# Performance work log

Measured on AMD Instinct MI355X. Metric: run time of the kernel, lower is better.

## Reference

```python
import jax, jax.numpy as jnp
import numpy as np

B, S, D, H, L = 32, 512, 256, 8, 3
HD = D // H
FFN = D // 2
SCALE_BASE = 512.0
EPS = 1e-5


def _gammas():
    return (1.0 - jnp.exp(jnp.linspace(np.log(1.0 / 32.0), np.log(1.0 / 512.0), H))).astype(jnp.float32)


def _xpos(x, downscale):
    # x: [..., S, hd]; XPOS rotary embedding with exponential length scaling
    s, hd = x.shape[-2], x.shape[-1]
    half = hd // 2
    scale = (jnp.arange(0, hd, 2, dtype=jnp.float32) + 0.4 * hd) / (1.4 * hd)  # [half]
    power = jnp.arange(s, dtype=jnp.float32)[:, None] / SCALE_BASE
    sm = scale[None, :] ** power  # [S, half]
    if downscale:
        sm = 1.0 / sm
    inv_freq = 1.0 / (10000.0 ** (jnp.arange(half, dtype=jnp.float32) / half))
    ang = jnp.arange(s, dtype=jnp.float32)[:, None] * inv_freq[None, :]  # [S, half]
    sin = jnp.repeat(jnp.sin(ang) * sm, 2, axis=-1)  # duplicate_interleave -> [S, hd]
    cos = jnp.repeat(jnp.cos(ang) * sm, 2, axis=-1)
    x1, x2 = x[..., ::2], x[..., 1::2]
    rot = jnp.stack((-x2, x1), axis=-1).reshape(x.shape)  # rotate_every_two
    return x * cos + rot * sin


def _layer_norm(x, w, b):
    mu = x.mean(-1, keepdims=True)
    var = ((x - mu) ** 2).mean(-1, keepdims=True)
    return (x - mu) / jnp.sqrt(var + EPS) * w + b


def _msr(X, WQ, WK, WV, WG, WO, gn_w, gn_b):
    # Multi-scale retention, parallel form. X: [B,S,D]; WQ/WK/WV: [H,D,HD]
    b, s, _ = X.shape
    Q = _xpos(jnp.einsum('bsd,hde->bhse', X, WQ), False)
    K = _xpos(jnp.einsum('bsd,hde->bhse', X, WK), True)
    V = jnp.einsum('bsd,hde->bhse', X, WV)
    n = jnp.arange(s)
    delta = (n[:, None] - n[None, :]).astype(jnp.float32)
    mask = n[:, None] >= n[None, :]
    g = _gammas()
    Dm = jnp.where(mask[None], g[:, None, None] ** delta[None], 0.0)  # [H,S,S]
    scores = jnp.einsum('bhse,bhte->bhst', Q, K) * Dm[None]  # [B,H,S,S]
    Y = jnp.einsum('bhst,bhte->bhse', scores, V)  # [B,H,S,HD]
    Y = jnp.moveaxis(Y, 1, 2)  # [B,S,H,HD] (= concat heads)
    # GroupNorm(heads, v_dim): normalize per (token, head) group
    mu = Y.mean(-1, keepdims=True)
    var = ((Y - mu) ** 2).mean(-1, keepdims=True)
    Yn = ((Y - mu) / jnp.sqrt(var + EPS)).reshape(b, s, D) * gn_w + gn_b
    G = X @ WG
    return (G * jax.nn.sigmoid(G) * Yn) @ WO


def setup_inputs() -> dict:
    key = jax.random.key(0)
    ks = jax.random.split(key, 10)
    inp = {
        'v': jax.random.randint(ks[0], (B, S), 0, 65, dtype=jnp.int64),
        'emb': jax.random.normal(ks[1], (65, D), dtype=jnp.float32),
        'WQ': jax.random.normal(ks[2], (L, H, D, HD), dtype=jnp.float32) / D,
        'WK': jax.random.normal(ks[3], (L, H, D, HD), dtype=jnp.float32) / D,
        'WV': jax.random.normal(ks[4], (L, H, D, HD), dtype=jnp.float32) / D,
        'WG': jax.random.normal(ks[5], (L, D, D), dtype=jnp.float32) / D,
        'WO': jax.random.normal(ks[6], (L, D, D), dtype=jnp.float32) / D,
        'gn_w': jnp.ones((L, D), jnp.float32),
        'gn_b': jnp.zeros((L, D), jnp.float32),
        'ln1_w': jnp.ones((L, D), jnp.float32),
        'ln1_b': jnp.zeros((L, D), jnp.float32),
        'ln2_w': jnp.ones((L, D), jnp.float32),
        'ln2_b': jnp.zeros((L, D), jnp.float32),
        'w1': jax.random.normal(ks[7], (L, D, FFN), dtype=jnp.float32) * (1.0 / np.sqrt(D)),
        'b1': jnp.zeros((L, FFN), jnp.float32),
        'w2': jax.random.normal(ks[8], (L, FFN, D), dtype=jnp.float32) * (1.0 / np.sqrt(FFN)),
        'b2': jnp.zeros((L, D), jnp.float32),
    }
    return inp


def reference(v, emb, WQ, WK, WV, WG, WO, gn_w, gn_b, ln1_w, ln1_b, ln2_w, ln2_b, w1, b1, w2, b2):
    emb = emb.at[0].set(0.0)  # padding_idx=0
    X = jax.nn.relu(emb[v])  # [B,S,D]
    for i in range(L):
        Y = _msr(_layer_norm(X, ln1_w[i], ln1_b[i]), WQ[i], WK[i], WV[i], WG[i], WO[i], gn_w[i], gn_b[i]) + X
        h = jax.nn.gelu(_layer_norm(Y, ln2_w[i], ln2_b[i]) @ w1[i] + b1[i], approximate=False)
        X = h @ w2[i] + b2[i] + Y
    return X
```

## Files before the change

### kernel.cpp

```cpp
#include <hip/hip_runtime.h>
#include <hip/hip_bf16.h>
#include <math.h>

#define BB 32
#define SS 512
#define DD 256
#define HH 8
#define HDIM 32
#define FFNN 128
#define NROWS (BB*SS)
#define NELEM (NROWS*DD)

using bf16 = __hip_bfloat16;
typedef __attribute__((ext_vector_type(8))) short short8;
typedef __attribute__((ext_vector_type(4))) short short4v;
typedef __attribute__((ext_vector_type(4))) float floatx4;
typedef unsigned int uint_al __attribute__((may_alias));

static __device__ __forceinline__ float bf2f(bf16 x) { return __bfloat162float(x); }
static __device__ __forceinline__ bf16  f2bf(float x) { return __float2bfloat16(x); }
static __device__ __forceinline__ short f2bfs(float x) {
    bf16 b = __float2bfloat16(x);
    return __builtin_bit_cast(short, b);
}

static __device__ __forceinline__ unsigned int cvtpk(float a, float b) {
    unsigned int r;
    asm("v_cvt_pk_bf16_f32 %0, %1, %2" : "=v"(r) : "v"(a), "v"(b));
    return r;
}
static __device__ __forceinline__ short4v mk4(unsigned int a, unsigned int b) {
    union { unsigned int u[2]; short4v s; } t;
    t.u[0] = a; t.u[1] = b;
    return t.s;
}
static __device__ __forceinline__ floatx4 mfma16(short4v a, short4v b, floatx4 c) {
#if __has_builtin(__builtin_amdgcn_mfma_f32_16x16x16bf16_1k)
    return __builtin_amdgcn_mfma_f32_16x16x16bf16_1k(a, b, c, 0, 0, 0);
#else
    asm("v_mfma_f32_16x16x16_bf16 %0, %1, %2, %0" : "+v"(c) : "v"(a), "v"(b));
    return c;
#endif
}

static __device__ __forceinline__ void gld_lds16(const void* g, void* l) {
    __builtin_amdgcn_global_load_lds(
        (const __attribute__((address_space(1))) void*)g,
        (__attribute__((address_space(3))) void*)l, 16, 0, 0);
}

__global__ void init_flag(int* flag) { *flag = 0; }
__global__ __launch_bounds__(256) void detect_v(const int* __restrict__ v, int* __restrict__ flag) {
    int i = blockIdx.x * 256 + threadIdx.x;
    if (v[2 * i + 1] != 0) atomicOr(flag, 1);
}

#define NQKVG (3*1024*256)
#define NWO   (3*256*256)
#define NW1   (3*128*256)
#define NW2   (3*256*128)
#define NXPT  (512*16)
#define NSETUP (NQKVG+NWO+NW1+NW2+NXPT)
__global__ __launch_bounds__(256) void setup_pack(const float* __restrict__ WQ, const float* __restrict__ WK,
                                                  const float* __restrict__ WV, const float* __restrict__ WG,
                                                  const float* __restrict__ WO, const float* __restrict__ w1,
                                                  const float* __restrict__ w2,
                                                  bf16* __restrict__ dQ, bf16* __restrict__ dO,
                                                  bf16* __restrict__ d1, bf16* __restrict__ d2,
                                                  float4* __restrict__ xpt) {
    int idx = blockIdx.x * 256 + threadIdx.x;
    if (idx < NQKVG) {
        int k = idx & 255, n = (idx >> 8) & 1023, l = idx >> 18;
        int seg = n >> 8, n8 = n & 255;
        float val;
        if (seg < 3) {
            const float* W = (seg == 0) ? WQ : (seg == 1) ? WK : WV;
            int h = n8 >> 5, e = n8 & 31;
            val = W[(((size_t)l * 8 + h) * 256 + k) * 32 + e];
        } else {
            val = WG[(size_t)l * 65536 + k * 256 + n8];
        }
        dQ[((size_t)l * 1024 + n) * 256 + k] = f2bf(val);
    } else if (idx < NQKVG + NWO) {
        int i = idx - NQKVG;
        int k = i & 255, n = (i >> 8) & 255, l = i >> 16;
        dO[((size_t)l * 256 + n) * 256 + k] = f2bf(WO[(size_t)l * 65536 + k * 256 + n]);
    } else if (idx < NQKVG + NWO + NW1) {
        int i = idx - NQKVG - NWO;
        int k = i & 255, n = (i >> 8) & 127, l = i >> 15;
        d1[((size_t)l * 128 + n) * 256 + k] = f2bf(w1[(size_t)l * 32768 + k * 128 + n]);
    } else if (idx < NQKVG + NWO + NW1 + NW2) {
        int i = idx - NQKVG - NWO - NW1;
        int k = i & 127, n = (i >> 7) & 255, l = i >> 15;
        d2[((size_t)l * 256 + n) * 128 + k] = f2bf(w2[(size_t)l * 32768 + k * 256 + n]);
    } else {
        int i = idx - NQKVG - NWO - NW1 - NW2;
        int jf = i & 15, s = i >> 4;
        float base = (2.0f * jf + 12.8f) / 44.8f;
        float sm = powf(base, (float)s * (1.0f / 512.0f));
        float ang = (float)s * powf(10000.0f, -(float)jf / 16.0f);
        float sn, cs;
        sincosf(ang, &sn, &cs);
        xpt[i] = float4{cs * sm, sn * sm, cs / sm, sn / sm};
    }
}

__global__ __launch_bounds__(256) void embed_ln_kernel(const int* __restrict__ v,
                                                       const float* __restrict__ emb,
                                                       const int* __restrict__ flag,
                                                       const float* __restrict__ w,
                                                       const float* __restrict__ b,
                                                       float* __restrict__ X,
                                                       short* __restrict__ Xn) {
    int row = blockIdx.x;
    int d = threadIdx.x;
    int tok = (*flag) ? v[row] : v[2 * row];
    float x = 0.0f;
    if (tok != 0) {
        x = emb[tok * DD + d];
        x = x > 0.0f ? x : 0.0f;
    }
    X[(size_t)row * DD + d] = x;
    float s1 = x, s2 = x * x;
    #pragma unroll
    for (int off = 1; off < 64; off <<= 1) {
        s1 += __shfl_xor(s1, off);
        s2 += __shfl_xor(s2, off);
    }
    __shared__ float p1[4], p2[4], st[2];
    int wid = threadIdx.x >> 6;
    if ((threadIdx.x & 63) == 0) { p1[wid] = s1; p2[wid] = s2; }
    __syncthreads();
    if (threadIdx.x == 0) {
        float t1 = p1[0] + p1[1] + p1[2] + p1[3];
        float t2 = p2[0] + p2[1] + p2[2] + p2[3];
        float mu = t1 * (1.0f / DD);
        float var = t2 * (1.0f / DD) - mu * mu;
        st[0] = mu; st[1] = rsqrtf(var + 1e-5f);
    }
    __syncthreads();
    Xn[(size_t)row * DD + d] = f2bfs((x - st[0]) * st[1] * w[d] + b[d]);
}

__global__ __launch_bounds__(256) void qkvg_gemm(const short* __restrict__ A,
                                                 const short* __restrict__ Bp,
                                                 const float4* __restrict__ xpt,
                                                 bf16* __restrict__ C) {
    __shared__ __align__(16) short Als[16 * 512];
    __shared__ __align__(16) short Bls[16 * 512];
    const int tid = threadIdx.x;
    const int wave = tid >> 6, lane = tid & 63, lo = lane & 15, quad = lane >> 4;
    const int wm = wave >> 1, wn = wave & 1;
    const int row0 = blockIdx.x * 128, col0 = blockIdx.y * 128;

    floatx4 acc[4][4];
    #pragma unroll
    for (int i = 0; i < 4; ++i)
        #pragma unroll
        for (int j = 0; j < 4; ++j) acc[i][j] = floatx4{0.f, 0.f, 0.f, 0.f};

    for (int k0 = 0; k0 < 256; k0 += 64) {
        #pragma unroll
        for (int t = 0; t < 4; ++t) {
            int grp = (wm * 4 + t) * 2 + wn;
            const short* ga = A + (size_t)(row0 + (wm * 4 + t) * 16 + lo) * 256
                            + k0 + (wn * 4 + quad) * 8;
            gld_lds16(ga, &Als[grp * 512]);
        }
        #pragma unroll
        for (int t = 0; t < 4; ++t) {
            int grp = (wn * 4 + t) * 2 + wm;
            const short* gb = Bp + (size_t)(col0 + (wn * 4 + t) * 16 + lo) * 256
                            + k0 + (wm * 4 + quad) * 8;
            gld_lds16(gb, &Bls[grp * 512]);
        }
        __syncthreads();
        #pragma unroll
        for (int kkgrp = 0; kkgrp < 2; ++kkgrp) {
            short8 af[4], bfr[4];
            #pragma unroll
            for (int t = 0; t < 4; ++t)
                af[t] = *(const short8*)(&Als[((wm * 4 + t) * 2 + kkgrp) * 512 + lane * 8]);
            #pragma unroll
            for (int t = 0; t < 4; ++t)
                bfr[t] = *(const short8*)(&Bls[((wn * 4 + t) * 2 + kkgrp) * 512 + lane * 8]);
            #pragma unroll
            for (int ti = 0; ti < 4; ++ti)
                #pragma unroll
                for (int tj = 0; tj < 4; ++tj)
                    acc[ti][tj] = __builtin_amdgcn_mfma_f32_16x16x32_bf16(af[ti], bfr[tj], acc[ti][tj], 0, 0, 0);
        }
        __syncthreads();
    }

    #pragma unroll
    for (int ti = 0; ti < 4; ++ti) {
        #pragma unroll
        for (int tj = 0; tj < 4; ++tj) {
            int colb = col0 + (wn * 4 + tj) * 16 + lo;
            int seg = colb >> 8;
            #pragma unroll
            for (int r = 0; r < 4; ++r) {
                int row = row0 + (wm * 4 + ti) * 16 + quad * 4 + r;
                float v = acc[ti][tj][r];
                if (seg < 2) {
                    int s = row & (SS - 1);
                    int jf = (colb & 31) >> 1;
                    float4 t = xpt[s * 16 + jf];
                    float cs = (seg == 0) ? t.x : t.z;
                    float sn = (seg == 0) ? t.y : t.w;
                    float p = __shfl_xor(v, 1);
                    v = (lo & 1) ? (v * cs + p * sn) : (v * cs - p * sn);
                }
                C[(size_t)row * 1024 + colb] = f2bf(v);
            }
        }
    }
}

__global__ __launch_bounds__(256) void wo_gemm(const short* __restrict__ A,
                                               const short* __restrict__ Bp,
                                               float* __restrict__ X,
                                               const float* __restrict__ lnw,
                                               const float* __restrict__ lnb,
                                               short* __restrict__ Out) {
    __shared__ __align__(16) short Als[4 * 512];
    __shared__ __align__(16) short Bls[4][8 * 512];
    __shared__ float Ssum[32][4], Ssq[32][4];
    const int tid = threadIdx.x;
    const int wave = tid >> 6, lane = tid & 63, lo = lane & 15, quad = lane >> 4;
    const int row0 = blockIdx.x * 32;
    const int colw0 = wave * 64;

    floatx4 acc[2][4];
    #pragma unroll
    for (int i = 0; i < 2; ++i)
        #pragma unroll
        for (int j = 0; j < 4; ++j) acc[i][j] = floatx4{0.f, 0.f, 0.f, 0.f};

    const short* Ab = A + (size_t)(row0 + (wave >> 1) * 16 + lo) * 1024 + ((wave & 1) * 4 + quad) * 8;
    const short* Bb = Bp + (size_t)(colw0 + lo) * 256 + quad * 8;

    for (int k0 = 0; k0 < 256; k0 += 64) {
        gld_lds16(Ab + k0, &Als[wave * 512]);
        #pragma unroll
        for (int t = 0; t < 4; ++t)
            #pragma unroll
            for (int kk = 0; kk < 2; ++kk)
                gld_lds16(Bb + (size_t)(t * 16) * 256 + k0 + kk * 32,
                          &Bls[wave][(t * 2 + kk) * 512]);
        __syncthreads();
        #pragma unroll
        for (int kk = 0; kk < 2; ++kk) {
            short8 af[2], bfr[4];
            #pragma unroll
            for (int t = 0; t < 2; ++t)
                af[t] = *(const short8*)(&Als[(t * 2 + kk) * 512 + lane * 8]);
            #pragma unroll
            for (int t = 0; t < 4; ++t)
                bfr[t] = *(const short8*)(&Bls[wave][(t * 2 + kk) * 512 + lane * 8]);
            #pragma unroll
            for (int ti = 0; ti < 2; ++ti)
                #pragma unroll
                for (int tj = 0; tj < 4; ++tj)
                    acc[ti][tj] = __builtin_amdgcn_mfma_f32_16x16x32_bf16(af[ti], bfr[tj], acc[ti][tj], 0, 0, 0);
        }
        __syncthreads();
    }

    float vv[2][4][4];
    #pragma unroll
    for (int ti = 0; ti < 2; ++ti)
        #pragma unroll
        for (int tj = 0; tj < 4; ++tj) {
            int colb = colw0 + tj * 16 + lo;
            #pragma unroll
            for (int r = 0; r < 4; ++r) {
                int row = row0 + ti * 16 + quad * 4 + r;
                float v = acc[ti][tj][r] + X[(size_t)row * DD + colb];
                X[(size_t)row * DD + colb] = v;
                vv[ti][tj][r] = v;
            }
        }
    #pragma unroll
    for (int ti = 0; ti < 2; ++ti)
        #pragma unroll
        for (int r = 0; r < 4; ++r) {
            float s1 = 0.f, s2 = 0.f;
            #pragma unroll
            for (int tj = 0; tj < 4; ++tj) {
                float v = vv[ti][tj][r];
                s1 += v; s2 += v * v;
            }
            #pragma unroll
            for (int off = 1; off < 16; off <<= 1) {
                s1 += __shfl_xor(s1, off);
                s2 += __shfl_xor(s2, off);
            }
            if (lo == 0) {
                int rl = ti * 16 + quad * 4 + r;
                Ssum[rl][wave] = s1;
                Ssq[rl][wave] = s2;
            }
        }
    __syncthreads();
    #pragma unroll
    for (int ti = 0; ti < 2; ++ti)
        #pragma unroll
        for (int r = 0; r < 4; ++r) {
            int rl = ti * 16 + quad * 4 + r;
            float t1 = Ssum[rl][0] + Ssum[rl][1] + Ssum[rl][2] + Ssum[rl][3];
            float t2 = Ssq[rl][0] + Ssq[rl][1] + Ssq[rl][2] + Ssq[rl][3];
            float mu = t1 * (1.0f / DD);
            float var = t2 * (1.0f / DD) - mu * mu;
            float rs = rsqrtf(var + 1e-5f);
            int row = row0 + rl;
            #pragma unroll
            for (int tj = 0; tj < 4; ++tj) {
                int colb = colw0 + tj * 16 + lo;
                Out[(size_t)row * DD + colb] =
                    f2bfs((vv[ti][tj][r] - mu) * rs * lnw[colb] + lnb[colb]);
            }
        }
}

#define HSTR 136
template<int DOLN>
__global__ __launch_bounds__(256) void ffn_fused(const short* __restrict__ Xn,
                                                 const short* __restrict__ W1p,
                                                 const float* __restrict__ b1,
                                                 const short* __restrict__ W2p,
                                                 const float* __restrict__ b2,
                                                 float* __restrict__ X,
                                                 const float* __restrict__ lnw,
                                                 const float* __restrict__ lnb,
                                                 short* __restrict__ Out) {
    __shared__ __align__(16) short Als[4 * 512];
    __shared__ __align__(16) short Bls[4][8 * 512];
    __shared__ __align__(16) short Hls[32 * HSTR];
    __shared__ float Ssum[32][4], Ssq[32][4];
    const int tid = threadIdx.x;
    const int wave = tid >> 6, lane = tid & 63, lo = lane & 15, quad = lane >> 4;
    const int row0 = blockIdx.x * 32;

    floatx4 a1[2][2];
    #pragma unroll
    for (int i = 0; i < 2; ++i) { a1[i][0] = floatx4{0,0,0,0}; a1[i][1] = floatx4{0,0,0,0}; }
    const short* Ab = Xn + (size_t)(row0 + (wave >> 1) * 16 + lo) * 256 + ((wave & 1) * 4 + quad) * 8;
    const short* Bb1 = W1p + (size_t)(wave * 32 + lo) * 256 + quad * 8;
    for (int k0 = 0; k0 < 256; k0 += 64) {
        gld_lds16(Ab + k0, &Als[wave * 512]);
        #pragma unroll
        for (int t = 0; t < 2; ++t)
            #pragma unroll
            for (int kk = 0; kk < 2; ++kk)
                gld_lds16(Bb1 + (size_t)(t * 16) * 256 + k0 + kk * 32,
                          &Bls[wave][(t * 2 + kk) * 512]);
        __syncthreads();
        #pragma unroll
        for (int kk = 0; kk < 2; ++kk) {
            short8 af[2], bfr[2];
            #pragma unroll
            for (int t = 0; t < 2; ++t)
                af[t] = *(const short8*)(&Als[(t * 2 + kk) * 512 + lane * 8]);
            #pragma unroll
            for (int t = 0; t < 2; ++t)
                bfr[t] = *(const short8*)(&Bls[wave][(t * 2 + kk) * 512 + lane * 8]);
            #pragma unroll
            for (int ti = 0; ti < 2; ++ti)
                #pragma unroll
                for (int tj = 0; tj < 2; ++tj)
                    a1[ti][tj] = __builtin_amdgcn_mfma_f32_16x16x32_bf16(af[ti], bfr[tj], a1[ti][tj], 0, 0, 0);
        }
        __syncthreads();
    }
    #pragma unroll
    for (int ti = 0; ti < 2; ++ti)
        #pragma unroll
        for (int tj = 0; tj < 2; ++tj) {
            int colb = wave * 32 + tj * 16 + lo;
            float bs = b1[colb];
            #pragma unroll
            for (int r = 0; r < 4; ++r) {
                int rl = ti * 16 + quad * 4 + r;
                float v = a1[ti][tj][r] + bs;
                v = 0.5f * v * (1.0f + erff(v * 0.70710678118f));
                Hls[rl * HSTR + colb] = f2bfs(v);
            }
        }

    floatx4 a2[2][4];
    #pragma unroll
    for (int i = 0; i < 2; ++i)
        #pragma unroll
        for (int j = 0; j < 4; ++j) a2[i][j] = floatx4{0,0,0,0};
    const short* Bb2 = W2p + (size_t)(wave * 64 + lo) * 128 + quad * 8;
    for (int k0 = 0; k0 < 128; k0 += 64) {
        #pragma unroll
        for (int t = 0; t < 4; ++t)
            #pragma unroll
            for (int kk = 0; kk < 2; ++kk)
                gld_lds16(Bb2 + (size_t)(t * 16) * 128 + k0 + kk * 32,
                          &Bls[wave][(t * 2 + kk) * 512]);
        __syncthreads();
        #pragma unroll
        for (int kk = 0; kk < 2; ++kk) {
            short8 af[2], bfr[4];
            #pragma unroll
            for (int t = 0; t < 2; ++t)
                af[t] = *(const short8*)(&Hls[(t * 16 + lo) * HSTR + k0 + kk * 32 + quad * 8]);
            #pragma unroll
            for (int t = 0; t < 4; ++t)
                bfr[t] = *(const short8*)(&Bls[wave][(t * 2 + kk) * 512 + lane * 8]);
            #pragma unroll
            for (int ti = 0; ti < 2; ++ti)
                #pragma unroll
                for (int tj = 0; tj < 4; ++tj)
                    a2[ti][tj] = __builtin_amdgcn_mfma_f32_16x16x32_bf16(af[ti], bfr[tj], a2[ti][tj], 0, 0, 0);
        }
        __syncthreads();
    }

    float vv[2][4][4];
    #pragma unroll
    for (int ti = 0; ti < 2; ++ti)
        #pragma unroll
        for (int tj = 0; tj < 4; ++tj) {
            int colb = wave * 64 + tj * 16 + lo;
            float bs = b2[colb];
            #pragma unroll
            for (int r = 0; r < 4; ++r) {
                int row = row0 + ti * 16 + quad * 4 + r;
                float v = a2[ti][tj][r] + bs + X[(size_t)row * DD + colb];
                X[(size_t)row * DD + colb] = v;
                vv[ti][tj][r] = v;
            }
        }
    if (!DOLN) return;
    #pragma unroll
    for (int ti = 0; ti < 2; ++ti)
        #pragma unroll
        for (int r = 0; r < 4; ++r) {
            float s1 = 0.f, s2 = 0.f;
            #pragma unroll
            for (int tj = 0; tj < 4; ++tj) {
                float v = vv[ti][tj][r];
                s1 += v; s2 += v * v;
            }
            #pragma unroll
            for (int off = 1; off < 16; off <<= 1) {
                s1 += __shfl_xor(s1, off);
                s2 += __shfl_xor(s2, off);
            }
            if (lo == 0) {
                int rl = ti * 16 + quad * 4 + r;
                Ssum[rl][wave] = s1;
                Ssq[rl][wave] = s2;
            }
        }
    __syncthreads();
    #pragma unroll
    for (int ti = 0; ti < 2; ++ti)
        #pragma unroll
        for (int r = 0; r < 4; ++r) {
            int rl = ti * 16 + quad * 4 + r;
            float t1 = Ssum[rl][0] + Ssum[rl][1] + Ssum[rl][2] + Ssum[rl][3];
            float t2 = Ssq[rl][0] + Ssq[rl][1] + Ssq[rl][2] + Ssq[rl][3];
            float mu = t1 * (1.0f / DD);
            float var = t2 * (1.0f / DD) - mu * mu;
            float rs = rsqrtf(var + 1e-5f);
            int row = row0 + rl;
            #pragma unroll
            for (int tj = 0; tj < 4; ++tj) {
                int colb = wave * 64 + tj * 16 + lo;
                Out[(size_t)row * DD + colb] =
                    f2bfs((vv[ti][tj][r] - mu) * rs * lnw[colb] + lnb[colb]);
            }
        }
}

#define VSTR 44
__global__ __launch_bounds__(256) void retention_mfma_kernel(bf16* __restrict__ QKVG,
                                                             const float* __restrict__ gnw,
                                                             const float* __restrict__ gnb) {
    __shared__ __align__(16) short Vt[4][32 * VSTR];
    const int wslot = threadIdx.x >> 6;
    const int lane = threadIdx.x & 63;
    const int gblk = blockIdx.x >> 6;
    const int qi = 15 - ((gblk & ~3) + (((gblk & 3) + (gblk >> 2)) & 3));
    const int bh = ((blockIdx.x & 63) << 2) | wslot;
    const int b = bh >> 3, h = bh & 7;
    const int q0 = qi * 32;
    const int lo = lane & 15, quad = lane >> 4;

    const float la0 = -3.46573590280f, la1 = -6.23832462504f;
    float gamma = 1.0f - expf(la0 + (float)h * (la1 - la0) / 7.0f);
    float lg2 = log2f(gamma);
    float g16i = exp2f(-16.0f * lg2);
    float g16p = exp2f(16.0f * lg2);
    float gi32 = exp2f(-32.0f * lg2);
    float wq[4], wq16[4], wqB[4];
    #pragma unroll
    for (int r = 0; r < 4; ++r) {
        wq[r]   = exp2f((float)(lo - 4 * quad - r) * lg2);
        wq16[r] = wq[r] * g16i;
        wqB[r]  = wq[r] * g16p;
    }
    float c = exp2f((float)q0 * lg2);

    const size_t base = (size_t)b * SS * 1024;
    const short* QKVGs = (const short*)QKVG;

    short8 qfA = *(const short8*)(QKVGs + base + (size_t)(q0 + lo) * 1024 + h * HDIM + quad * 8);
    short8 qfB = *(const short8*)(QKVGs + base + (size_t)(q0 + 16 + lo) * 1024 + h * HDIM + quad * 8);

    floatx4 oA0 = {0,0,0,0}, oA1 = {0,0,0,0}, oB0 = {0,0,0,0}, oB1 = {0,0,0,0};
    short* Vw = Vt[wslot];
    const int nch = qi + 1;

    for (int ch = 0; ch < nch; ++ch) {
        const int t0 = ch * 32;
        const short* Kb = QKVGs + base + 256 + h * HDIM + quad * 8;
        short8 kf0 = *(const short8*)(Kb + (size_t)(t0 + lo) * 1024);
        short8 kf1 = *(const short8*)(Kb + (size_t)(t0 + 16 + lo) * 1024);
        {
            const int r = lane >> 2, dcol = (lane & 3) * 8;
            const short* Vg = QKVGs + base + 512 + h * HDIM + dcol;
            uint4 u1 = *(const uint4*)(Vg + (size_t)(t0 + r) * 1024);
            uint4 u2 = *(const uint4*)(Vg + (size_t)(t0 + 16 + r) * 1024);
            uint_al* W1 = (uint_al*)(Vw + r * VSTR + dcol);
            uint_al* W2 = (uint_al*)(Vw + (16 + r) * VSTR + dcol);
            W1[0] = u1.x; W1[1] = u1.y; W1[2] = u1.z; W1[3] = u1.w;
            W2[0] = u2.x; W2[1] = u2.y; W2[2] = u2.z; W2[3] = u2.w;
        }
        const floatx4 z = {0,0,0,0};
        floatx4 sA0 = __builtin_amdgcn_mfma_f32_16x16x32_bf16(kf0, qfA, z, 0, 0, 0);
        floatx4 sA1 = __builtin_amdgcn_mfma_f32_16x16x32_bf16(kf1, qfA, z, 0, 0, 0);
        floatx4 sB0 = __builtin_amdgcn_mfma_f32_16x16x32_bf16(kf0, qfB, z, 0, 0, 0);
        floatx4 sB1 = __builtin_amdgcn_mfma_f32_16x16x32_bf16(kf1, qfB, z, 0, 0, 0);

        float m0[4], m1[4], mB[4];
        #pragma unroll
        for (int r = 0; r < 4; ++r) {
            m0[r] = c * wq[r];
            m1[r] = c * wq16[r];
            mB[r] = c * wqB[r];
        }
        if (ch == qi) {
            #pragma unroll
            for (int r = 0; r < 4; ++r) {
                if (lo < 4 * quad + r) m0[r] = 0.0f;
                m1[r] = 0.0f;
            }
        }
        c *= gi32;

        unsigned int pa0 = cvtpk(sA0[0] * m0[0], sA0[1] * m0[1]);
        unsigned int pa1 = cvtpk(sA0[2] * m0[2], sA0[3] * m0[3]);
        unsigned int pa2 = cvtpk(sA1[0] * m1[0], sA1[1] * m1[1]);
        unsigned int pa3 = cvtpk(sA1[2] * m1[2], sA1[3] * m1[3]);
        unsigned int pb0 = cvtpk(sB0[0] * mB[0], sB0[1] * mB[1]);
        unsigned int pb1 = cvtpk(sB0[2] * mB[2], sB0[3] * mB[3]);
        unsigned int pb2 = cvtpk(sB1[0] * m0[0], sB1[1] * m0[1]);
        unsigned int pb3 = cvtpk(sB1[2] * m0[2], sB1[3] * m0[3]);
        short4v pA0 = mk4(pa0, pa1), pA1 = mk4(pa2, pa3);
        short4v pB0 = mk4(pb0, pb1), pB1 = mk4(pb2, pb3);

        short4v v00, v01, v10, v11;
        #pragma unroll
        for (int j = 0; j < 4; ++j) {
            v00[j] = Vw[(4 * quad + j) * VSTR + lo];
            v01[j] = Vw[(16 + 4 * quad + j) * VSTR + lo];
            v10[j] = Vw[(4 * quad + j) * VSTR + 16 + lo];
            v11[j] = Vw[(16 + 4 * quad + j) * VSTR + 16 + lo];
        }
        oA0 = mfma16(pA0, v00, oA0);
        oA0 = mfma16(pA1, v01, oA0);
        oA1 = mfma16(pA0, v10, oA1);
        oA1 = mfma16(pA1, v11, oA1);
        oB0 = mfma16(pB0, v00, oB0);
        oB0 = mfma16(pB1, v01, oB0);
        oB1 = mfma16(pB0, v10, oB1);
        oB1 = mfma16(pB1, v11, oB1);
    }

    float gw0 = gnw[h * HDIM + lo], gw1 = gnw[h * HDIM + 16 + lo];
    float gb0 = gnb[h * HDIM + lo], gb1 = gnb[h * HDIM + 16 + lo];
    bf16* QK = QKVG;
    #pragma unroll
    for (int sub = 0; sub < 2; ++sub) {
        floatx4 o0 = sub ? oB0 : oA0;
        floatx4 o1 = sub ? oB1 : oA1;
        int qbase = q0 + sub * 16;
        #pragma unroll
        for (int r = 0; r < 4; ++r) {
            float y0 = o0[r], y1 = o1[r];
            float s = y0 + y1, ss = y0 * y0 + y1 * y1;
            #pragma unroll
            for (int off = 1; off < 16; off <<= 1) {
                s  += __shfl_xor(s, off);
                ss += __shfl_xor(ss, off);
            }
            float mu = s * (1.0f / HDIM);
            float var = ss * (1.0f / HDIM) - mu * mu;
            float rstd = rsqrtf(var + 1e-5f);
            int q = qbase + quad * 4 + r;
            size_t rowb = base + (size_t)q * 1024;
            float g0 = bf2f(QK[rowb + 768 + h * HDIM + lo]);
            float g1 = bf2f(QK[rowb + 768 + h * HDIM + 16 + lo]);
            float t0v = g0 / (1.0f + expf(-g0)) * ((y0 - mu) * rstd * gw0 + gb0);
            float t1v = g1 / (1.0f + expf(-g1)) * ((y1 - mu) * rstd * gw1 + gb1);
            QK[rowb + h * HDIM + lo]      = f2bf(t0v);
            QK[rowb + h * HDIM + 16 + lo] = f2bf(t1v);
        }
    }
}

extern "C" void kernel_launch(void* const* d_in, const int* in_sizes, int n_in,
                              void* d_out, int out_size, void* d_ws, size_t ws_size,
                              hipStream_t stream) {
    const int*   v    = (const int*)d_in[0];
    const float* emb  = (const float*)d_in[1];
    const float* WQ   = (const float*)d_in[2];
    const float* WK   = (const float*)d_in[3];
    const float* WV   = (const float*)d_in[4];
    const float* WG   = (const float*)d_in[5];
    const float* WO   = (const float*)d_in[6];
    const float* gn_w = (const float*)d_in[7];
    const float* gn_b = (const float*)d_in[8];
    const float* ln1w = (const float*)d_in[9];
    const float* ln1b = (const float*)d_in[10];
    const float* ln2w = (const float*)d_in[11];
    const float* ln2b = (const float*)d_in[12];
    const float* w1   = (const float*)d_in[13];
    const float* b1   = (const float*)d_in[14];
    const float* w2   = (const float*)d_in[15];
    const float* b2   = (const float*)d_in[16];

    float* X = (float*)d_out;

    float* base  = (float*)d_ws;
    int*   flag  = (int*)base;
    short* Xn    = (short*)(base + 16);
    bf16*  QKVG  = (bf16*)(Xn + (size_t)NROWS * 256);
    bf16*  WqkvgP = QKVG + (size_t)NROWS * 1024;
    bf16*  WoP   = WqkvgP + 3 * 1024 * 256;
    bf16*  W1P   = WoP + 3 * 256 * 256;
    bf16*  W2P   = W1P + 3 * 128 * 256;
    float4* xpt  = (float4*)(W2P + 3 * 256 * 128);

    init_flag<<<1, 1, 0, stream>>>(flag);
    detect_v<<<32, 256, 0, stream>>>(v, flag);
    setup_pack<<<NSETUP / 256, 256, 0, stream>>>(WQ, WK, WV, WG, WO, w1, w2,
                                                 WqkvgP, WoP, W1P, W2P, xpt);
    embed_ln_kernel<<<NROWS, 256, 0, stream>>>(v, emb, flag, ln1w, ln1b, X, Xn);

    for (int i = 0; i < 3; ++i) {
        qkvg_gemm<<<dim3(128, 8), 256, 0, stream>>>(Xn,
                                                    (const short*)(WqkvgP + (size_t)i * 1024 * 256),
                                                    xpt, QKVG);
        retention_mfma_kernel<<<1024, 256, 0, stream>>>(QKVG, gn_w + i * DD, gn_b + i * DD);
        wo_gemm<<<NROWS / 32, 256, 0, stream>>>((const short*)QKVG,
                                                (const short*)(WoP + (size_t)i * 256 * 256),
                                                X, ln2w + i * DD, ln2b + i * DD, Xn);
        if (i < 2)
            ffn_fused<1><<<NROWS / 32, 256, 0, stream>>>(Xn,
                                                         (const short*)(W1P + (size_t)i * 128 * 256),
                                                         b1 + i * FFNN,
                                                         (const short*)(W2P + (size_t)i * 256 * 128),
                                                         b2 + i * DD, X,
                                                         ln1w + (i + 1) * DD, ln1b + (i + 1) * DD, Xn);
        else
            ffn_fused<0><<<NROWS / 32, 256, 0, stream>>>(Xn,
                                                         (const short*)(W1P + (size_t)i * 128 * 256),
                                                         b1 + i * FFNN,
                                                         (const short*)(W2P + (size_t)i * 256 * 128),
                                                         b2 + i * DD, X,
                                                         nullptr, nullptr, nullptr);
    }
}
```

Baseline: 396.4 us.

## Fuse WO projection, LayerNorm and FFN into one kernel per layer

Merges the WO GEMM kernel and the FFN kernel into a single kernel per row block. The post-residual LayerNorm output stays in LDS as the FFN input, and the residual stays in registers. This removes one launch per layer, the global round trip of the normalized activations, and a reread of X. In exchange, LDS use per block grows (an extra 32x264 bf16 buffer) and register pressure rises, which may lower occupancy.

```diff
diff --git a/kernel.cpp b/kernel.cpp
--- a/kernel.cpp
+++ b/kernel.cpp
@@ -218,14 +218,25 @@
     }
 }
 
-__global__ __launch_bounds__(256) void wo_gemm(const short* __restrict__ A,
-                                               const short* __restrict__ Bp,
-                                               float* __restrict__ X,
-                                               const float* __restrict__ lnw,
-                                               const float* __restrict__ lnb,
-                                               short* __restrict__ Out) {
+#define HS2 264
+#define HSTR 136
+template<int DOLN>
+__global__ __launch_bounds__(256) void wo_ffn_fused(const short* __restrict__ A,
+                                                    const short* __restrict__ Wo,
+                                                    const short* __restrict__ W1p,
+                                                    const float* __restrict__ b1,
+                                                    const short* __restrict__ W2p,
+                                                    const float* __restrict__ b2,
+                                                    float* __restrict__ X,
+                                                    const float* __restrict__ ln2w,
+                                                    const float* __restrict__ ln2b,
+                                                    const float* __restrict__ ln1w,
+                                                    const float* __restrict__ ln1b,
+                                                    short* __restrict__ Xn) {
     __shared__ __align__(16) short Als[4 * 512];
     __shared__ __align__(16) short Bls[4][8 * 512];
+    __shared__ __align__(16) short Hn[32 * HS2];
+    __shared__ __align__(16) short Hf[32 * HSTR];
     __shared__ float Ssum[32][4], Ssq[32][4];
     const int tid = threadIdx.x;
     const int wave = tid >> 6, lane = tid & 63, lo = lane & 15, quad = lane >> 4;
@@ -239,7 +250,7 @@
         for (int j = 0; j < 4; ++j) acc[i][j] = floatx4{0.f, 0.f, 0.f, 0.f};
 
     const short* Ab = A + (size_t)(row0 + (wave >> 1) * 16 + lo) * 1024 + ((wave & 1) * 4 + quad) * 8;
-    const short* Bb = Bp + (size_t)(colw0 + lo) * 256 + quad * 8;
+    const short* Bb = Wo + (size_t)(colw0 + lo) * 256 + quad * 8;
 
     for (int k0 = 0; k0 < 256; k0 += 64) {
         gld_lds16(Ab + k0, &Als[wave * 512]);
@@ -277,11 +288,141 @@
             #pragma unroll
             for (int r = 0; r < 4; ++r) {
                 int row = row0 + ti * 16 + quad * 4 + r;
-                float v = acc[ti][tj][r] + X[(size_t)row * DD + colb];
+                vv[ti][tj][r] = acc[ti][tj][r] + X[(size_t)row * DD + colb];
+            }
+        }
+    #pragma unroll
+    for (int ti = 0; ti < 2; ++ti)
+        #pragma unroll
+        for (int r = 0; r < 4; ++r) {
+            float s1 = 0.f, s2 = 0.f;
+            #pragma unroll
+            for (int tj = 0; tj < 4; ++tj) {
+                float v = vv[ti][tj][r];
+                s1 += v; s2 += v * v;
+            }
+            #pragma unroll
+            for (int off = 1; off < 16; off <<= 1) {
+                s1 += __shfl_xor(s1, off);
+                s2 += __shfl_xor(s2, off);
+            }
+            if (lo == 0) {
+                int rl = ti * 16 + quad * 4 + r;
+                Ssum[rl][wave] = s1;
+                Ssq[rl][wave] = s2;
+            }
+        }
+    __syncthreads();
+    #pragma unroll
+    for (int ti = 0; ti < 2; ++ti)
+        #pragma unroll
+        for (int r = 0; r < 4; ++r) {
+            int rl = ti * 16 + quad * 4 + r;
+            float t1 = Ssum[rl][0] + Ssum[rl][1] + Ssum[rl][2] + Ssum[rl][3];
+            float t2 = Ssq[rl][0] + Ssq[rl][1] + Ssq[rl][2] + Ssq[rl][3];
+            float mu = t1 * (1.0f / DD);
+            float var = t2 * (1.0f / DD) - mu * mu;
+            float rs = rsqrtf(var + 1e-5f);
+            #pragma unroll
+            for (int tj = 0; tj < 4; ++tj) {
+                int colb = colw0 + tj * 16 + lo;
+                Hn[rl * HS2 + colb] =
+                    f2bfs((vv[ti][tj][r] - mu) * rs * ln2w[colb] + ln2b[colb]);
+            }
+        }
+    __syncthreads();
+
+    floatx4 a1[2][2];
+    #pragma unroll
+    for (int i = 0; i < 2; ++i) { a1[i][0] = floatx4{0,0,0,0}; a1[i][1] = floatx4{0,0,0,0}; }
+    const short* Bb1 = W1p + (size_t)(wave * 32 + lo) * 256 + quad * 8;
+    for (int k0 = 0; k0 < 256; k0 += 64) {
+        #pragma unroll
+        for (int t = 0; t < 2; ++t)
+            #pragma unroll
+            for (int kk = 0; kk < 2; ++kk)
+                gld_lds16(Bb1 + (size_t)(t * 16) * 256 + k0 + kk * 32,
+                          &Bls[wave][(t * 2 + kk) * 512]);
+        __syncthreads();
+        #pragma unroll
+        for (int kk = 0; kk < 2; ++kk) {
+            short8 af[2], bfr[2];
+            #pragma unroll
+            for (int t = 0; t < 2; ++t)
+                af[t] = *(const short8*)(&Hn[(t * 16 + lo) * HS2 + k0 + kk * 32 + quad * 8]);
+            #pragma unroll
+            for (int t = 0; t < 2; ++t)
+                bfr[t] = *(const short8*)(&Bls[wave][(t * 2 + kk) * 512 + lane * 8]);
+            #pragma unroll
+            for (int ti = 0; ti < 2; ++ti)
+                #pragma unroll
+                for (int tj = 0; tj < 2; ++tj)
+                    a1[ti][tj] = __builtin_amdgcn_mfma_f32_16x16x32_bf16(af[ti], bfr[tj], a1[ti][tj], 0, 0, 0);
+        }
+        __syncthreads();
+    }
+    #pragma unroll
+    for (int ti = 0; ti < 2; ++ti)
+        #pragma unroll
+        for (int tj = 0; tj < 2; ++tj) {
+            int colb = wave * 32 + tj * 16 + lo;
+            float bs = b1[colb];
+            #pragma unroll
+            for (int r = 0; r < 4; ++r) {
+                int rl = ti * 16 + quad * 4 + r;
+                float v = a1[ti][tj][r] + bs;
+                v = 0.5f * v * (1.0f + erff(v * 0.70710678118f));
+                Hf[rl * HSTR + colb] = f2bfs(v);
+            }
+        }
+
+    floatx4 a2[2][4];
+    #pragma unroll
+    for (int i = 0; i < 2; ++i)
+        #pragma unroll
+        for (int j = 0; j < 4; ++j) a2[i][j] = floatx4{0,0,0,0};
+    const short* Bb2 = W2p + (size_t)(colw0 + lo) * 128 + quad * 8;
+    for (int k0 = 0; k0 < 128; k0 += 64) {
+        #pragma unroll
+        for (int t = 0; t < 4; ++t)
+            #pragma unroll
+            for (int kk = 0; kk < 2; ++kk)
+                gld_lds16(Bb2 + (size_t)(t * 16) * 128 + k0 + kk * 32,
+                          &Bls[wave][(t * 2 + kk) * 512]);
+        __syncthreads();
+        #pragma unroll
+        for (int kk = 0; kk < 2; ++kk) {
+            short8 af[2], bfr[4];
+            #pragma unroll
+            for (int t = 0; t < 2; ++t)
+                af[t] = *(const short8*)(&Hf[(t * 16 + lo) * HSTR + k0 + kk * 32 + quad * 8]);
+            #pragma unroll
+            for (int t = 0; t < 4; ++t)
+                bfr[t] = *(const short8*)(&Bls[wave][(t * 2 + kk) * 512 + lane * 8]);
+            #pragma unroll
+            for (int ti = 0; ti < 2; ++ti)
+                #pragma unroll
+                for (int tj = 0; tj < 4; ++tj)
+                    a2[ti][tj] = __builtin_amdgcn_mfma_f32_16x16x32_bf16(af[ti], bfr[tj], a2[ti][tj], 0, 0, 0);
+        }
+        __syncthreads();
+    }
+
+    #pragma unroll
+    for (int ti = 0; ti < 2; ++ti)
+        #pragma unroll
+        for (int tj = 0; tj < 4; ++tj) {
+            int colb = colw0 + tj * 16 + lo;
+            float bs = b2[colb];
+            #pragma unroll
+            for (int r = 0; r < 4; ++r) {
+                int row = row0 + ti * 16 + quad * 4 + r;
+                float v = a2[ti][tj][r] + bs + vv[ti][tj][r];
                 X[(size_t)row * DD + colb] = v;
                 vv[ti][tj][r] = v;
             }
         }
+    if (!DOLN) return;
     #pragma unroll
     for (int ti = 0; ti < 2; ++ti)
         #pragma unroll
@@ -318,163 +459,8 @@
             #pragma unroll
             for (int tj = 0; tj < 4; ++tj) {
                 int colb = colw0 + tj * 16 + lo;
-                Out[(size_t)row * DD + colb] =
-                    f2bfs((vv[ti][tj][r] - mu) * rs * lnw[colb] + lnb[colb]);
-            }
-        }
-}
-
-#define HSTR 136
-template<int DOLN>
-__global__ __launch_bounds__(256) void ffn_fused(const short* __restrict__ Xn,
-                                                 const short* __restrict__ W1p,
-                                                 const float* __restrict__ b1,
-                                                 const short* __restrict__ W2p,
-                                                 const float* __restrict__ b2,
-                                                 float* __restrict__ X,
-                                                 const float* __restrict__ lnw,
-                                                 const float* __restrict__ lnb,
-                                                 short* __restrict__ Out) {
-    __shared__ __align__(16) short Als[4 * 512];
-    __shared__ __align__(16) short Bls[4][8 * 512];
-    __shared__ __align__(16) short Hls[32 * HSTR];
-    __shared__ float Ssum[32][4], Ssq[32][4];
-    const int tid = threadIdx.x;
-    const int wave = tid >> 6, lane = tid & 63, lo = lane & 15, quad = lane >> 4;
-    const int row0 = blockIdx.x * 32;
-
-    floatx4 a1[2][2];
-    #pragma unroll
-    for (int i = 0; i < 2; ++i) { a1[i][0] = floatx4{0,0,0,0}; a1[i][1] = floatx4{0,0,0,0}; }
-    const short* Ab = Xn + (size_t)(row0 + (wave >> 1) * 16 + lo) * 256 + ((wave & 1) * 4 + quad) * 8;
-    const short* Bb1 = W1p + (size_t)(wave * 32 + lo) * 256 + quad * 8;
-    for (int k0 = 0; k0 < 256; k0 += 64) {
-        gld_lds16(Ab + k0, &Als[wave * 512]);
-        #pragma unroll
-        for (int t = 0; t < 2; ++t)
-            #pragma unroll
-            for (int kk = 0; kk < 2; ++kk)
-                gld_lds16(Bb1 + (size_t)(t * 16) * 256 + k0 + kk * 32,
-                          &Bls[wave][(t * 2 + kk) * 512]);
-        __syncthreads();
-        #pragma unroll
-        for (int kk = 0; kk < 2; ++kk) {
-            short8 af[2], bfr[2];
-            #pragma unroll
-            for (int t = 0; t < 2; ++t)
-                af[t] = *(const short8*)(&Als[(t * 2 + kk) * 512 + lane * 8]);
-            #pragma unroll
-            for (int t = 0; t < 2; ++t)
-                bfr[t] = *(const short8*)(&Bls[wave][(t * 2 + kk) * 512 + lane * 8]);
-            #pragma unroll
-            for (int ti = 0; ti < 2; ++ti)
-                #pragma unroll
-                for (int tj = 0; tj < 2; ++tj)
-                    a1[ti][tj] = __builtin_amdgcn_mfma_f32_16x16x32_bf16(af[ti], bfr[tj], a1[ti][tj], 0, 0, 0);
-        }
-        __syncthreads();
-    }
-    #pragma unroll
-    for (int ti = 0; ti < 2; ++ti)
-        #pragma unroll
-        for (int tj = 0; tj < 2; ++tj) {
-            int colb = wave * 32 + tj * 16 + lo;
-            float bs = b1[colb];
-            #pragma unroll
-            for (int r = 0; r < 4; ++r) {
-                int rl = ti * 16 + quad * 4 + r;
-                float v = a1[ti][tj][r] + bs;
-                v = 0.5f * v * (1.0f + erff(v * 0.70710678118f));
-                Hls[rl * HSTR + colb] = f2bfs(v);
-            }
-        }
-
-    floatx4 a2[2][4];
-    #pragma unroll
-    for (int i = 0; i < 2; ++i)
-        #pragma unroll
-        for (int j = 0; j < 4; ++j) a2[i][j] = floatx4{0,0,0,0};
-    const short* Bb2 = W2p + (size_t)(wave * 64 + lo) * 128 + quad * 8;
-    for (int k0 = 0; k0 < 128; k0 += 64) {
-        #pragma unroll
-        for (int t = 0; t < 4; ++t)
-            #pragma unroll
-            for (int kk = 0; kk < 2; ++kk)
-                gld_lds16(Bb2 + (size_t)(t * 16) * 128 + k0 + kk * 32,
-                          &Bls[wave][(t * 2 + kk) * 512]);
-        __syncthreads();
-        #pragma unroll
-        for (int kk = 0; kk < 2; ++kk) {
-            short8 af[2], bfr[4];
-            #pragma unroll
-            for (int t = 0; t < 2; ++t)
-                af[t] = *(const short8*)(&Hls[(t * 16 + lo) * HSTR + k0 + kk * 32 + quad * 8]);
-            #pragma unroll
-            for (int t = 0; t < 4; ++t)
-                bfr[t] = *(const short8*)(&Bls[wave][(t * 2 + kk) * 512 + lane * 8]);
-            #pragma unroll
-            for (int ti = 0; ti < 2; ++ti)
-                #pragma unroll
-                for (int tj = 0; tj < 4; ++tj)
-                    a2[ti][tj] = __builtin_amdgcn_mfma_f32_16x16x32_bf16(af[ti], bfr[tj], a2[ti][tj], 0, 0, 0);
-        }
-        __syncthreads();
-    }
-
-    float vv[2][4][4];
-    #pragma unroll
-    for (int ti = 0; ti < 2; ++ti)
-        #pragma unroll
-        for (int tj = 0; tj < 4; ++tj) {
-            int colb = wave * 64 + tj * 16 + lo;
-            float bs = b2[colb];
-            #pragma unroll
-            for (int r = 0; r < 4; ++r) {
-                int row = row0 + ti * 16 + quad * 4 + r;
-                float v = a2[ti][tj][r] + bs + X[(size_t)row * DD + colb];
-                X[(size_t)row * DD + colb] = v;
-                vv[ti][tj][r] = v;
-            }
-        }
-    if (!DOLN) return;
-    #pragma unroll
-    for (int ti = 0; ti < 2; ++ti)
-        #pragma unroll
-        for (int r = 0; r < 4; ++r) {
-            float s1 = 0.f, s2 = 0.f;
-            #pragma unroll
-            for (int tj = 0; tj < 4; ++tj) {
-                float v = vv[ti][tj][r];
-                s1 += v; s2 += v * v;
-            }
-            #pragma unroll
-            for (int off = 1; off < 16; off <<= 1) {
-                s1 += __shfl_xor(s1, off);
-                s2 += __shfl_xor(s2, off);
-            }
-            if (lo == 0) {
-                int rl = ti * 16 + quad * 4 + r;
-                Ssum[rl][wave] = s1;
-                Ssq[rl][wave] = s2;
-            }
-        }
-    __syncthreads();
-    #pragma unroll
-    for (int ti = 0; ti < 2; ++ti)
-        #pragma unroll
-        for (int r = 0; r < 4; ++r) {
-            int rl = ti * 16 + quad * 4 + r;
-            float t1 = Ssum[rl][0] + Ssum[rl][1] + Ssum[rl][2] + Ssum[rl][3];
-            float t2 = Ssq[rl][0] + Ssq[rl][1] + Ssq[rl][2] + Ssq[rl][3];
-            float mu = t1 * (1.0f / DD);
-            float var = t2 * (1.0f / DD) - mu * mu;
-            float rs = rsqrtf(var + 1e-5f);
-            int row = row0 + rl;
-            #pragma unroll
-            for (int tj = 0; tj < 4; ++tj) {
-                int colb = wave * 64 + tj * 16 + lo;
-                Out[(size_t)row * DD + colb] =
-                    f2bfs((vv[ti][tj][r] - mu) * rs * lnw[colb] + lnb[colb]);
+                Xn[(size_t)row * DD + colb] =
+                    f2bfs((vv[ti][tj][r] - mu) * rs * ln1w[colb] + ln1b[colb]);
             }
         }
 }
@@ -660,22 +646,23 @@
                                                     (const short*)(WqkvgP + (size_t)i * 1024 * 256),
                                                     xpt, QKVG);
         retention_mfma_kernel<<<1024, 256, 0, stream>>>(QKVG, gn_w + i * DD, gn_b + i * DD);
-        wo_gemm<<<NROWS / 32, 256, 0, stream>>>((const short*)QKVG,
-                                                (const short*)(WoP + (size_t)i * 256 * 256),
-                                                X, ln2w + i * DD, ln2b + i * DD, Xn);
         if (i < 2)
-            ffn_fused<1><<<NROWS / 32, 256, 0, stream>>>(Xn,
-                                                         (const short*)(W1P + (size_t)i * 128 * 256),
-                                                         b1 + i * FFNN,
-                                                         (const short*)(W2P + (size_t)i * 256 * 128),
-                                                         b2 + i * DD, X,
-                                                         ln1w + (i + 1) * DD, ln1b + (i + 1) * DD, Xn);
+            wo_ffn_fused<1><<<NROWS / 32, 256, 0, stream>>>((const short*)QKVG,
+                                                            (const short*)(WoP + (size_t)i * 256 * 256),
+                                                            (const short*)(W1P + (size_t)i * 128 * 256),
+                                                            b1 + i * FFNN,
+                                                            (const short*)(W2P + (size_t)i * 256 * 128),
+                                                            b2 + i * DD, X,
+                                                            ln2w + i * DD, ln2b + i * DD,
+                                                            ln1w + (i + 1) * DD, ln1b + (i + 1) * DD, Xn);
         else
-            ffn_fused<0><<<NROWS / 32, 256, 0, stream>>>(Xn,
-                                                         (const short*)(W1P + (size_t)i * 128 * 256),
-                                                         b1 + i * FFNN,
-                                                         (const short*)(W2P + (size_t)i * 256 * 128),
-                                                         b2 + i * DD, X,
-                                                         nullptr, nullptr, nullptr);
-    }
-}
+            wo_ffn_fused<0><<<NROWS / 32, 256, 0, stream>>>((const short*)QKVG,
+                                                            (const short*)(WoP + (size_t)i * 256 * 256),
+                                                            (const short*)(W1P + (size_t)i * 128 * 256),
+                                                            b1 + i * FFNN,
+                                                            (const short*)(W2P + (size_t)i * 256 * 128),
+                                                            b2 + i * DD, X,
+                                                            ln2w + i * DD, ln2b + i * DD,
+                                                            nullptr, nullptr, nullptr);
+    }
+}
```

After: 360.3 us. 9.1% less time.
